# Kernel tuning notes

Hardware: AMD Instinct MI355X
Metric: run time of the kernel (lower is better)

The kernel has to match this reference:

```python
import jax, jax.numpy as jnp
import numpy as np

H, W, F, V, D = 1024, 1024, 100000, 50000, 32


def setup_inputs() -> dict:
    key = jax.random.key(0)
    k1, k2, k3, k4 = jax.random.split(key, 4)
    pix_to_face = jax.random.randint(k1, (H, W), 0, F, dtype=jnp.int64 if jax.config.read('jax_enable_x64') else jnp.int32)
    bg = jax.random.uniform(k2, (H, W)) < 0.1
    pix_to_face = jnp.where(bg, -1, pix_to_face)
    bary = jax.random.uniform(k2, (H, W, 3), dtype=jnp.float32)
    bary_coords = bary / jnp.sum(bary, axis=-1, keepdims=True)  # barycentric: sums to 1
    faces = jax.random.randint(k3, (F, 3), 0, V, dtype=pix_to_face.dtype)
    attributes = jax.random.normal(k4, (V, D), dtype=jnp.float32)
    return {"pix_to_face": pix_to_face, "bary_coords": bary_coords,
            "faces": faces, "attributes": attributes}


def reference(pix_to_face, bary_coords, faces, attributes):
    # faces[pix_to_face]: (H, W, 3) vertex indices (torch -1 wraps to last face)
    vertices_idx = jnp.take(faces, pix_to_face, axis=0, mode='wrap')
    # attributes[vertices_idx]: (H, W, 3, D)
    vertex_attribute = jnp.take(attributes, vertices_idx, axis=0, mode='wrap')
    # barycentric weighted sum over the 3 face vertices -> (H, W, D)
    attribute_map = jnp.einsum('hwk,hwkd->hwd', bary_coords, vertex_attribute)
    mask = pix_to_face != -1
    return attribute_map, mask
```

## Files before the change

kernel.cpp:

```cpp
#include <hip/hip_runtime.h>
#include <hip/hip_bf16.h>


__global__ __launch_bounds__(256) void Renderer_interp_kernel(
    const int* __restrict__ pix,
    const float* __restrict__ bary,
    const int* __restrict__ faces,
    const float* __restrict__ attr,
    float* __restrict__ out,
    float* __restrict__ mask,
    int npix, int F)
{
    int tid = blockIdx.x * blockDim.x + threadIdx.x;
    int p = tid >> 3;
    int t = tid & 7;
    if (p >= npix) return;

    int fraw = pix[p];
    int f = (fraw < 0) ? (fraw + F) : fraw;

    int base = 3 * f;
    int v0 = faces[base + 0];
    int v1 = faces[base + 1];
    int v2 = faces[base + 2];

    float w0 = bary[3 * p + 0];
    float w1 = bary[3 * p + 1];
    float w2 = bary[3 * p + 2];

    const float4* A = reinterpret_cast<const float4*>(attr);
    float4 r0 = A[v0 * 8 + t];
    float4 r1 = A[v1 * 8 + t];
    float4 r2 = A[v2 * 8 + t];

    float4 o;
    o.x = w0 * r0.x + w1 * r1.x + w2 * r2.x;
    o.y = w0 * r0.y + w1 * r1.y + w2 * r2.y;
    o.z = w0 * r0.z + w1 * r1.z + w2 * r2.z;
    o.w = w0 * r0.w + w1 * r1.w + w2 * r2.w;

    reinterpret_cast<float4*>(out)[p * 8 + t] = o;

    if (t == 0) {
        mask[p] = (fraw != -1) ? 1.0f : 0.0f;
    }
}

extern "C" void kernel_launch(void* const* d_in, const int* in_sizes, int n_in,
                              void* d_out, int out_size, void* d_ws, size_t ws_size,
                              hipStream_t stream) {
    const int*   pix   = (const int*)d_in[0];
    const float* bary  = (const float*)d_in[1];
    const int*   faces = (const int*)d_in[2];
    const float* attr  = (const float*)d_in[3];

    int npix = in_sizes[0];
    int F    = in_sizes[2] / 3;

    float* out  = (float*)d_out;
    float* mask = (float*)d_out + (size_t)npix * 32;

    int total = npix * 8;
    int block = 256;
    int grid = (total + block - 1) / block;
    Renderer_interp_kernel<<<grid, block, 0, stream>>>(pix, bary, faces, attr,
                                                       out, mask, npix, F);
}
```

Measured before the change: 65.57 us.

## Split pixel channels across paired blocks and use nontemporal streaming loads/stores

Each block now covers 64 pixels with 4 threads per pixel, handling one half (16 channels) of the output. The two halves of a pixel go to adjacent blocks selected by the low bit of the block index. Streaming inputs (pix, bary) and outputs (out, mask) use nontemporal loads and stores, so the L2 cache is left mostly to the randomly gathered faces and attribute rows. In exchange, the face indices, pixel index and weights are loaded twice per pixel, once in each half-block.

```diff
diff --git a/kernel.cpp b/kernel.cpp
--- a/kernel.cpp
+++ b/kernel.cpp
@@ -1,6 +1,8 @@
 #include <hip/hip_runtime.h>
 #include <hip/hip_bf16.h>
 
+
+typedef float fvec4 __attribute__((ext_vector_type(4)));
 
 __global__ __launch_bounds__(256) void Renderer_interp_kernel(
     const int* __restrict__ pix,
@@ -11,12 +13,16 @@
     float* __restrict__ mask,
     int npix, int F)
 {
-    int tid = blockIdx.x * blockDim.x + threadIdx.x;
-    int p = tid >> 3;
-    int t = tid & 7;
+    int h    = blockIdx.x & 1;
+    int pblk = blockIdx.x >> 1;
+    int lp   = threadIdx.x >> 2;
+    int q    = threadIdx.x & 3;
+    int p    = pblk * 64 + lp;
     if (p >= npix) return;
 
-    int fraw = pix[p];
+    int t = h * 4 + q;
+
+    int fraw = __builtin_nontemporal_load(&pix[p]);
     int f = (fraw < 0) ? (fraw + F) : fraw;
 
     int base = 3 * f;
@@ -24,25 +30,22 @@
     int v1 = faces[base + 1];
     int v2 = faces[base + 2];
 
-    float w0 = bary[3 * p + 0];
-    float w1 = bary[3 * p + 1];
-    float w2 = bary[3 * p + 2];
+    float w0 = __builtin_nontemporal_load(&bary[3 * p + 0]);
+    float w1 = __builtin_nontemporal_load(&bary[3 * p + 1]);
+    float w2 = __builtin_nontemporal_load(&bary[3 * p + 2]);
 
-    const float4* A = reinterpret_cast<const float4*>(attr);
-    float4 r0 = A[v0 * 8 + t];
-    float4 r1 = A[v1 * 8 + t];
-    float4 r2 = A[v2 * 8 + t];
+    const fvec4* A = reinterpret_cast<const fvec4*>(attr);
+    fvec4 r0 = A[v0 * 8 + t];
+    fvec4 r1 = A[v1 * 8 + t];
+    fvec4 r2 = A[v2 * 8 + t];
 
-    float4 o;
-    o.x = w0 * r0.x + w1 * r1.x + w2 * r2.x;
-    o.y = w0 * r0.y + w1 * r1.y + w2 * r2.y;
-    o.z = w0 * r0.z + w1 * r1.z + w2 * r2.z;
-    o.w = w0 * r0.w + w1 * r1.w + w2 * r2.w;
+    fvec4 o = w0 * r0 + w1 * r1 + w2 * r2;
 
-    reinterpret_cast<float4*>(out)[p * 8 + t] = o;
+    fvec4* O = reinterpret_cast<fvec4*>(out);
+    __builtin_nontemporal_store(o, &O[(size_t)p * 8 + t]);
 
-    if (t == 0) {
-        mask[p] = (fraw != -1) ? 1.0f : 0.0f;
+    if (h == 0 && q == 0) {
+        __builtin_nontemporal_store((fraw != -1) ? 1.0f : 0.0f, &mask[p]);
     }
 }
 
@@ -60,9 +63,7 @@
     float* out  = (float*)d_out;
     float* mask = (float*)d_out + (size_t)npix * 32;
 
-    int total = npix * 8;
-    int block = 256;
-    int grid = (total + block - 1) / block;
-    Renderer_interp_kernel<<<grid, block, 0, stream>>>(pix, bary, faces, attr,
-                                                       out, mask, npix, F);
+    int nblk = ((npix + 63) / 64) * 2;
+    Renderer_interp_kernel<<<nblk, 256, 0, stream>>>(pix, bary, faces, attr,
+                                                     out, mask, npix, F);
 }
```

After: 106.5 us. 62.4% more time.

## Slice attribute table into column chunks and process one slice per block

Applied to the files above, without the earlier changes.

Adds a pre-pass that rearranges the attribute table into four 8-float column slices stored contiguously, then launches the interpolation with each block handling one slice for 128 pixels. This shrinks the working set each block gathers from (about 1.6 MB per slice), so random vertex gathers should hit cache more often. Output and mask stores become nontemporal. In exchange it adds an extra kernel launch and a full copy of the table each call, and the pixel, bary and face reads are repeated four times. The original kernel stays as a fallback when workspace is too small.

```diff
diff --git a/kernel.cpp b/kernel.cpp
--- a/kernel.cpp
+++ b/kernel.cpp
@@ -2,18 +2,36 @@
 #include <hip/hip_bf16.h>
 
 
-__global__ __launch_bounds__(256) void Renderer_interp_kernel(
+typedef float fvec4 __attribute__((ext_vector_type(4)));
+
+__global__ __launch_bounds__(256) void Renderer_transpose_kernel(
+    const fvec4* __restrict__ A,
+    fvec4* __restrict__ W,
+    int V)
+{
+    int tid = blockIdx.x * blockDim.x + threadIdx.x;
+    if (tid >= V * 8) return;
+    int v = tid >> 3;
+    int c = tid & 7;
+    int s = c >> 1;
+    int j = c & 1;
+    W[((size_t)s * V + v) * 2 + j] = A[tid];
+}
+
+__global__ __launch_bounds__(256) void Renderer_interp_sliced_kernel(
     const int* __restrict__ pix,
     const float* __restrict__ bary,
     const int* __restrict__ faces,
-    const float* __restrict__ attr,
+    const fvec4* __restrict__ W,
     float* __restrict__ out,
     float* __restrict__ mask,
-    int npix, int F)
+    int npix, int F, int V)
 {
-    int tid = blockIdx.x * blockDim.x + threadIdx.x;
-    int p = tid >> 3;
-    int t = tid & 7;
+    int s     = blockIdx.x & 3;
+    int pblk  = blockIdx.x >> 2;
+    int lp    = threadIdx.x >> 1;
+    int j     = threadIdx.x & 1;
+    int p     = pblk * 128 + lp;
     if (p >= npix) return;
 
     int fraw = pix[p];
@@ -28,22 +46,40 @@
     float w1 = bary[3 * p + 1];
     float w2 = bary[3 * p + 2];
 
-    const float4* A = reinterpret_cast<const float4*>(attr);
-    float4 r0 = A[v0 * 8 + t];
-    float4 r1 = A[v1 * 8 + t];
-    float4 r2 = A[v2 * 8 + t];
+    const fvec4* S = W + (size_t)s * V * 2;
+    fvec4 r0 = S[v0 * 2 + j];
+    fvec4 r1 = S[v1 * 2 + j];
+    fvec4 r2 = S[v2 * 2 + j];
 
-    float4 o;
-    o.x = w0 * r0.x + w1 * r1.x + w2 * r2.x;
-    o.y = w0 * r0.y + w1 * r1.y + w2 * r2.y;
-    o.z = w0 * r0.z + w1 * r1.z + w2 * r2.z;
-    o.w = w0 * r0.w + w1 * r1.w + w2 * r2.w;
+    fvec4 o = w0 * r0 + w1 * r1 + w2 * r2;
 
-    reinterpret_cast<float4*>(out)[p * 8 + t] = o;
+    fvec4* O = reinterpret_cast<fvec4*>(out);
+    __builtin_nontemporal_store(o, &O[(size_t)p * 8 + s * 2 + j]);
 
-    if (t == 0) {
-        mask[p] = (fraw != -1) ? 1.0f : 0.0f;
+    if (s == 0 && j == 0) {
+        __builtin_nontemporal_store((fraw != -1) ? 1.0f : 0.0f, &mask[p]);
     }
+}
+
+__global__ __launch_bounds__(256) void Renderer_interp_kernel(
+    const int* __restrict__ pix, const float* __restrict__ bary,
+    const int* __restrict__ faces, const float* __restrict__ attr,
+    float* __restrict__ out, float* __restrict__ mask, int npix, int F)
+{
+    int tid = blockIdx.x * blockDim.x + threadIdx.x;
+    int p = tid >> 3;
+    int t = tid & 7;
+    if (p >= npix) return;
+    int fraw = pix[p];
+    int f = (fraw < 0) ? (fraw + F) : fraw;
+    int base = 3 * f;
+    int v0 = faces[base + 0], v1 = faces[base + 1], v2 = faces[base + 2];
+    float w0 = bary[3 * p + 0], w1 = bary[3 * p + 1], w2 = bary[3 * p + 2];
+    const fvec4* A = reinterpret_cast<const fvec4*>(attr);
+    fvec4 r0 = A[v0 * 8 + t], r1 = A[v1 * 8 + t], r2 = A[v2 * 8 + t];
+    fvec4 o = w0 * r0 + w1 * r1 + w2 * r2;
+    reinterpret_cast<fvec4*>(out)[(size_t)p * 8 + t] = o;
+    if (t == 0) mask[p] = (fraw != -1) ? 1.0f : 0.0f;
 }
 
 extern "C" void kernel_launch(void* const* d_in, const int* in_sizes, int n_in,
@@ -56,13 +92,24 @@
 
     int npix = in_sizes[0];
     int F    = in_sizes[2] / 3;
+    int V    = in_sizes[3] / 32;
 
     float* out  = (float*)d_out;
     float* mask = (float*)d_out + (size_t)npix * 32;
 
-    int total = npix * 8;
-    int block = 256;
-    int grid = (total + block - 1) / block;
-    Renderer_interp_kernel<<<grid, block, 0, stream>>>(pix, bary, faces, attr,
-                                                       out, mask, npix, F);
+    size_t need = (size_t)V * 32 * sizeof(float);
+
+    if (ws_size >= need) {
+        fvec4* W = (fvec4*)d_ws;
+        int nthr = V * 8;
+        Renderer_transpose_kernel<<<(nthr + 255) / 256, 256, 0, stream>>>(
+            (const fvec4*)attr, W, V);
+        int nblk = ((npix + 127) / 128) * 4;
+        Renderer_interp_sliced_kernel<<<nblk, 256, 0, stream>>>(
+            pix, bary, faces, W, out, mask, npix, F, V);
+    } else {
+        int total = npix * 8;
+        Renderer_interp_kernel<<<(total + 255) / 256, 256, 0, stream>>>(
+            pix, bary, faces, attr, out, mask, npix, F);
+    }
 }
```

Measured after the change: 131.1 us. +100.0%, slower.
